# Kernel tuning notes

Measured on AMD Instinct MI355X. Metric: run time of the kernel, lower is better.

## Reference

```python
import jax, jax.numpy as jnp
import numpy as np

NUM_HEADS = 12
DIM = 1536
HEAD_DIM = DIM // NUM_HEADS
ROPE_BASE = 10000.0


def _alibi_slopes(n):
    import math
    def pow2_slopes(m):
        start = 2.0 ** (-(2.0 ** (-(math.log2(m) - 3))))
        return [start * (start ** i) for i in range(m)]
    if math.log2(n).is_integer():
        s = pow2_slopes(n)
    else:
        c = 2 ** math.floor(math.log2(n))
        s = pow2_slopes(c) + pow2_slopes(2 * c)[0::2][: n - c]
    return jnp.asarray(np.array(s, dtype=np.float32))


def _rope_tables(seq_len, head_dim, dtype):
    inv_freq = 1.0 / (ROPE_BASE ** (jnp.arange(0, head_dim, 2, dtype=jnp.float32) / head_dim))
    t = jnp.arange(seq_len, dtype=jnp.float32)
    freqs = jnp.outer(t, inv_freq)  # [S, head_dim/2]
    return jnp.cos(freqs).astype(dtype), jnp.sin(freqs).astype(dtype)


def _apply_rope(t, cos, sin):
    # t: [B,H,S,hd]; cos/sin: [S, hd/2] -> interleaved rotation
    te, to = t[..., 0::2], t[..., 1::2]
    rot = jnp.stack([te * cos - to * sin, te * sin + to * cos], axis=-1)
    return rot.reshape(t.shape)


def setup_inputs() -> dict:
    key = jax.random.key(0)
    ks = jax.random.split(key, 9)
    B, S, D = 2, 2048, DIM
    w_scale = 1.0 / np.sqrt(D)
    return {
        "x": jax.random.normal(ks[0], (B, S, D), dtype=jnp.float32),
        "Wq": jax.random.normal(ks[1], (D, D), dtype=jnp.float32) * w_scale,
        "bq": jnp.zeros((D,), dtype=jnp.float32),
        "Wk": jax.random.normal(ks[2], (D, D), dtype=jnp.float32) * w_scale,
        "bk": jnp.zeros((D,), dtype=jnp.float32),
        "Wv": jax.random.normal(ks[3], (D, D), dtype=jnp.float32) * w_scale,
        "bv": jnp.zeros((D,), dtype=jnp.float32),
        "Wo": jax.random.normal(ks[4], (D, D), dtype=jnp.float32) * w_scale,
        "bo": jnp.zeros((D,), dtype=jnp.float32),
    }


def reference(x, Wq, bq, Wk, bk, Wv, bv, Wo, bo):
    B, S, D = x.shape
    H, hd = NUM_HEADS, D // NUM_HEADS
    scale = hd ** -0.5

    def proj(W, b):
        # nn.Linear: x @ W.T + b ; reshape to [B,H,S,hd]
        y = jnp.einsum("bsd,ed->bse", x, W) + b
        return y.reshape(B, S, H, hd).transpose(0, 2, 1, 3)

    q, k, v = proj(Wq, bq), proj(Wk, bk), proj(Wv, bv)

    cos, sin = _rope_tables(S, hd, x.dtype)
    q = _apply_rope(q, cos, sin)
    k = _apply_rope(k, cos, sin)

    scores = jnp.einsum("bhqd,bhkd->bhqk", q, k) * scale
    slopes = _alibi_slopes(H)  # [H]
    # original bias: slopes * arange(seq_len) broadcast over key positions
    scores = scores + slopes[None, :, None, None] * jnp.arange(S, dtype=x.dtype)[None, None, None, :]

    attn = jax.nn.softmax(scores, axis=-1)  # dropout is identity at eval
    out = jnp.einsum("bhqk,bhkd->bhqd", attn, v)
    out = out.transpose(0, 2, 1, 3).reshape(B, S, D)
    return jnp.einsum("bsd,ed->bse", out, Wo) + bo
```

## Files before the change

### kernel.cpp

```cpp
#include <hip/hip_runtime.h>
#include <math.h>

#define S_LEN   2048
#define NHEADS  12
#define HD      128
#define DMODEL  1536
#define NBATCH  2

typedef __bf16 bf16x8 __attribute__((ext_vector_type(8)));
typedef float  f32x4  __attribute__((ext_vector_type(4)));
typedef unsigned short u16x8 __attribute__((ext_vector_type(8)));

__constant__ float c_slopes[NHEADS] = {
    0.5f, 0.25f, 0.125f, 0.0625f, 0.03125f, 0.015625f, 0.0078125f, 0.00390625f,
    0.70710678118654752f, 0.35355339059327379f,
    0.17677669529663689f, 0.08838834764831845f
};

__device__ __forceinline__ unsigned short f2bf(float x) {
    unsigned int u = __float_as_uint(x);
    u += 0x7FFFu + ((u >> 16) & 1u);
    return (unsigned short)(u >> 16);
}
__device__ __forceinline__ float bf2f(unsigned short h) {
    return __uint_as_float(((unsigned int)h) << 16);
}
__device__ __forceinline__ void splitf(float v, unsigned short &h, unsigned short &l) {
    h = f2bf(v);
    l = f2bf(v - bf2f(h));
}
__device__ __forceinline__ f32x4 mfma16(bf16x8 a, bf16x8 b, f32x4 c) {
    return __builtin_amdgcn_mfma_f32_16x16x32_bf16(a, b, c, 0, 0, 0);
}

__global__ void rope_table_kernel(float* __restrict__ cosT, float* __restrict__ sinT) {
    const int s = blockIdx.x;
    const int i = threadIdx.x;
    double inv = exp(-((double)i / 64.0) * 9.210340371976184);
    float argf = (float)s * (float)inv;
    double a = (double)argf;
    cosT[s * 64 + i] = (float)cos(a);
    sinT[s * 64 + i] = (float)sin(a);
}

__global__ __launch_bounds__(256)
void conv_hl_kernel(const float* __restrict__ src,
                    unsigned short* __restrict__ dh,
                    unsigned short* __restrict__ dl, int n8)
{
    int idx = blockIdx.x * 256 + threadIdx.x;
    if (idx >= n8) return;
    const float4* s = (const float4*)src + (size_t)idx * 2;
    float4 a = s[0], b = s[1];
    u16x8 hv, lv;
    unsigned short th, tl;
    splitf(a.x, th, tl); hv[0] = th; lv[0] = tl;
    splitf(a.y, th, tl); hv[1] = th; lv[1] = tl;
    splitf(a.z, th, tl); hv[2] = th; lv[2] = tl;
    splitf(a.w, th, tl); hv[3] = th; lv[3] = tl;
    splitf(b.x, th, tl); hv[4] = th; lv[4] = tl;
    splitf(b.y, th, tl); hv[5] = th; lv[5] = tl;
    splitf(b.z, th, tl); hv[6] = th; lv[6] = tl;
    splitf(b.w, th, tl); hv[7] = th; lv[7] = tl;
    *(u16x8*)(dh + (size_t)idx * 8) = hv;
    *(u16x8*)(dl + (size_t)idx * 8) = lv;
}

__global__ __launch_bounds__(256, 4)
void transpose_vt_kernel(const unsigned short* __restrict__ inH,
                         const unsigned short* __restrict__ inL,
                         unsigned short* __restrict__ outH,
                         unsigned short* __restrict__ outL)
{
    __shared__ unsigned short Th[64 * 65], Tl[64 * 65];
    const int tid = threadIdx.x;
    const int sx = blockIdx.x * 64, dx = blockIdx.y * 64;
    const int bh = blockIdx.z;
    const size_t ibase = (size_t)bh * S_LEN * HD;
    const size_t obase = (size_t)bh * HD * S_LEN;

#pragma unroll
    for (int t = 0; t < 2; t++) {
        int srow = (tid >> 3) + 32 * t;
        int c8 = tid & 7;
        u16x8 vh = *(const u16x8*)(inH + ibase + (size_t)(sx + srow) * HD + dx + c8 * 8);
        u16x8 vl = *(const u16x8*)(inL + ibase + (size_t)(sx + srow) * HD + dx + c8 * 8);
#pragma unroll
        for (int j = 0; j < 8; j++) {
            Th[(c8 * 8 + j) * 65 + srow] = vh[j];
            Tl[(c8 * 8 + j) * 65 + srow] = vl[j];
        }
    }
    __syncthreads();
#pragma unroll
    for (int t = 0; t < 2; t++) {
        int drow = (tid >> 3) + 32 * t;
        int c8 = tid & 7;
        u16x8 vh, vl;
#pragma unroll
        for (int j = 0; j < 8; j++) {
            vh[j] = Th[drow * 65 + c8 * 8 + j];
            vl[j] = Tl[drow * 65 + c8 * 8 + j];
        }
        *(u16x8*)(outH + obase + (size_t)(dx + drow) * S_LEN + sx + c8 * 8) = vh;
        *(u16x8*)(outL + obase + (size_t)(dx + drow) * S_LEN + sx + c8 * 8) = vl;
    }
}

#define BM 128
#define BN 128
#define BK 32
#define LDT 40

__global__ __launch_bounds__(256, 2)
void gemm_hl_kernel(const unsigned short* __restrict__ Agh, const unsigned short* __restrict__ Agl,
                    const unsigned short* __restrict__ Bgh, const unsigned short* __restrict__ Bgl,
                    int M, int N, int K,
                    float* __restrict__ outF, const float* __restrict__ bO,
                    unsigned short* __restrict__ Qh, unsigned short* __restrict__ Ql,
                    unsigned short* __restrict__ Kh, unsigned short* __restrict__ Kl,
                    unsigned short* __restrict__ Vh, unsigned short* __restrict__ Vl,
                    const float* __restrict__ bq, const float* __restrict__ bk,
                    const float* __restrict__ bv,
                    const float* __restrict__ cosT, const float* __restrict__ sinT,
                    int mode)
{
    __shared__ unsigned short Ah[BM * LDT], Al[BM * LDT];
    __shared__ unsigned short Bh[BN * LDT], Bl[BN * LDT];

    const int tid  = threadIdx.x;
    const int lane = tid & 63;
    const int wid  = tid >> 6;
    const int wm   = wid >> 1, wn = wid & 1;
    const int m0   = blockIdx.x * BM, n0 = blockIdx.y * BN;
    const int l15  = lane & 15, l4 = lane >> 4;
    const int kq   = l4 * 8;

    const int srow = tid >> 1, skc = (tid & 1) * 16;
    const size_t abase = (size_t)(m0 + srow) * K + skc;
    const size_t bbase = (size_t)(n0 + srow) * K + skc;

    f32x4 acc[4][4] = {};

    u16x8 pah0 = *(const u16x8*)(Agh + abase);
    u16x8 pah1 = *(const u16x8*)(Agh + abase + 8);
    u16x8 pal0 = *(const u16x8*)(Agl + abase);
    u16x8 pal1 = *(const u16x8*)(Agl + abase + 8);
    u16x8 pbh0 = *(const u16x8*)(Bgh + bbase);
    u16x8 pbh1 = *(const u16x8*)(Bgh + bbase + 8);
    u16x8 pbl0 = *(const u16x8*)(Bgl + bbase);
    u16x8 pbl1 = *(const u16x8*)(Bgl + bbase + 8);

    const int KT = K / BK;
    for (int kt = 0; kt < KT; ++kt) {
        __syncthreads();
        *(u16x8*)&Ah[srow * LDT + skc]     = pah0;
        *(u16x8*)&Ah[srow * LDT + skc + 8] = pah1;
        *(u16x8*)&Al[srow * LDT + skc]     = pal0;
        *(u16x8*)&Al[srow * LDT + skc + 8] = pal1;
        *(u16x8*)&Bh[srow * LDT + skc]     = pbh0;
        *(u16x8*)&Bh[srow * LDT + skc + 8] = pbh1;
        *(u16x8*)&Bl[srow * LDT + skc]     = pbl0;
        *(u16x8*)&Bl[srow * LDT + skc + 8] = pbl1;
        __syncthreads();

        if (kt + 1 < KT) {
            size_t ao = abase + (size_t)(kt + 1) * BK;
            size_t bo2 = bbase + (size_t)(kt + 1) * BK;
            pah0 = *(const u16x8*)(Agh + ao);
            pah1 = *(const u16x8*)(Agh + ao + 8);
            pal0 = *(const u16x8*)(Agl + ao);
            pal1 = *(const u16x8*)(Agl + ao + 8);
            pbh0 = *(const u16x8*)(Bgh + bo2);
            pbh1 = *(const u16x8*)(Bgh + bo2 + 8);
            pbl0 = *(const u16x8*)(Bgl + bo2);
            pbl1 = *(const u16x8*)(Bgl + bo2 + 8);
        }

        bf16x8 ah[4], al[4], bh[4], bl[4];
#pragma unroll
        for (int mi = 0; mi < 4; mi++) {
            int r = wm * 64 + mi * 16 + l15;
            ah[mi] = *(const bf16x8*)&Ah[r * LDT + kq];
            al[mi] = *(const bf16x8*)&Al[r * LDT + kq];
        }
#pragma unroll
        for (int ni = 0; ni < 4; ni++) {
            int r = wn * 64 + ni * 16 + l15;
            bh[ni] = *(const bf16x8*)&Bh[r * LDT + kq];
            bl[ni] = *(const bf16x8*)&Bl[r * LDT + kq];
        }
        __builtin_amdgcn_s_setprio(1);
#pragma unroll
        for (int mi = 0; mi < 4; mi++) {
#pragma unroll
            for (int ni = 0; ni < 4; ni++) {
                acc[mi][ni] = mfma16(ah[mi], bh[ni], acc[mi][ni]);
                acc[mi][ni] = mfma16(ah[mi], bl[ni], acc[mi][ni]);
                acc[mi][ni] = mfma16(al[mi], bh[ni], acc[mi][ni]);
            }
        }
        __builtin_amdgcn_s_setprio(0);
    }

#pragma unroll
    for (int ni = 0; ni < 4; ni++) {
        int col = n0 + wn * 64 + ni * 16 + l15;
        float bvv;
        unsigned short *dh = nullptr, *dl = nullptr;
        int colL = col, dorope = 0;
        if (mode == 0) {
            bvv = bO[col];
        } else {
            int which = col / 1536;
            colL = col - which * 1536;
            const float* bias = (which == 0) ? bq : (which == 1) ? bk : bv;
            dh = (which == 0) ? Qh : (which == 1) ? Kh : Vh;
            dl = (which == 0) ? Ql : (which == 1) ? Kl : Vl;
            dorope = (which < 2);
            bvv = bias[colL];
        }
        int hcol = colL >> 7;
        int d    = colL & (HD - 1);
#pragma unroll
        for (int mi = 0; mi < 4; mi++) {
#pragma unroll
            for (int r = 0; r < 4; r++) {
                int row = m0 + wm * 64 + mi * 16 + l4 * 4 + r;
                float v = acc[mi][ni][r] + bvv;
                if (mode == 0) {
                    outF[(size_t)row * N + col] = v;
                } else {
                    int bb = row >> 11;
                    int ss = row & (S_LEN - 1);
                    if (dorope) {
                        float p  = __shfl_xor(v, 1);
                        float cc = cosT[ss * 64 + (d >> 1)];
                        float sn = sinT[ss * 64 + (d >> 1)];
                        v = (d & 1) ? fmaf(p, sn, v * cc) : fmaf(-p, sn, v * cc);
                    }
                    unsigned short hh, ll;
                    splitf(v, hh, ll);
                    size_t o = ((size_t)(bb * NHEADS + hcol) * S_LEN + ss) * HD + d;
                    dh[o] = hh;
                    dl[o] = ll;
                }
            }
        }
    }
}

#define QB  64
#define KB  32
#define LKD 136
#define LVD 40
#define LPD 40

__global__ __launch_bounds__(256, 3)
void flash_kernel(const unsigned short* __restrict__ Qh, const unsigned short* __restrict__ Ql,
                  const unsigned short* __restrict__ Kh, const unsigned short* __restrict__ Kl,
                  const unsigned short* __restrict__ VTh, const unsigned short* __restrict__ VTl,
                  unsigned short* __restrict__ AOh, unsigned short* __restrict__ AOl)
{
    __shared__ unsigned short Ksh[KB * LKD], Ksl[KB * LKD];
    __shared__ unsigned short Vth[HD * LVD], Vtl[HD * LVD];
    __shared__ unsigned short Psh[4 * 16 * LPD], Psl[4 * 16 * LPD];

    const int tid  = threadIdx.x, lane = tid & 63, wid = tid >> 6;
    const int l15  = lane & 15, l4 = lane >> 4;
    const int kq   = l4 * 8;
    const int qt   = blockIdx.x, bh = blockIdx.y;
    const int b    = bh / NHEADS, h = bh % NHEADS;
    const float slope = c_slopes[h];
    const float scale = 0.088388347648318447f;

    const size_t base  = (size_t)bh * S_LEN * HD;
    const size_t vbase = (size_t)bh * HD * S_LEN;

    bf16x8 qfh[4], qfl[4];
    {
        const int qrow = qt * QB + wid * 16 + l15;
#pragma unroll
        for (int ks = 0; ks < 4; ks++) {
            size_t o = base + (size_t)qrow * HD + ks * 32 + kq;
            qfh[ks] = *(const bf16x8*)(Qh + o);
            qfl[ks] = *(const bf16x8*)(Ql + o);
        }
    }

    float m_r[4], l_r[4];
#pragma unroll
    for (int r = 0; r < 4; r++) { m_r[r] = -1e30f; l_r[r] = 0.0f; }
    f32x4 oacc[8] = {};

    unsigned short* Pmh = &Psh[wid * 16 * LPD];
    unsigned short* Pml = &Psl[wid * 16 * LPD];

    for (int it = 0; it < S_LEN / KB; ++it) {
        const int kt = (S_LEN / KB - 1) - it;
        __syncthreads();
#pragma unroll
        for (int i = 0; i < 2; i++) {
            int u = tid + 256 * i;
            int row = u >> 4, c8 = u & 15;
            size_t g = base + (size_t)(kt * KB + row) * HD + c8 * 8;
            *(u16x8*)&Ksh[row * LKD + c8 * 8] = *(const u16x8*)(Kh + g);
            *(u16x8*)&Ksl[row * LKD + c8 * 8] = *(const u16x8*)(Kl + g);
        }
#pragma unroll
        for (int i = 0; i < 2; i++) {
            int u = tid + 256 * i;
            int row = (u >> 2) & 127;
            int c = u & 3;
            size_t g = vbase + (size_t)row * S_LEN + kt * KB + c * 8;
            *(u16x8*)&Vth[row * LVD + c * 8] = *(const u16x8*)(VTh + g);
            *(u16x8*)&Vtl[row * LVD + c * 8] = *(const u16x8*)(VTl + g);
        }
        __syncthreads();

        f32x4 sc[2] = {};
        __builtin_amdgcn_s_setprio(1);
#pragma unroll
        for (int ks = 0; ks < 4; ks++) {
#pragma unroll
            for (int nf = 0; nf < 2; nf++) {
                int krow = nf * 16 + l15;
                bf16x8 kh = *(const bf16x8*)&Ksh[krow * LKD + ks * 32 + kq];
                bf16x8 kl = *(const bf16x8*)&Ksl[krow * LKD + ks * 32 + kq];
                sc[nf] = mfma16(qfh[ks], kh, sc[nf]);
                sc[nf] = mfma16(qfh[ks], kl, sc[nf]);
                sc[nf] = mfma16(qfl[ks], kh, sc[nf]);
            }
        }
        __builtin_amdgcn_s_setprio(0);

        float mnew[4];
        int grow = 0;
        const float bias0 = slope * (float)(kt * KB + l15);
        const float bias1 = slope * (float)(kt * KB + 16 + l15);
#pragma unroll
        for (int r = 0; r < 4; r++) {
            float s0 = fmaf(sc[0][r], scale, bias0);
            float s1 = fmaf(sc[1][r], scale, bias1);
            sc[0][r] = s0;
            sc[1][r] = s1;
            float mx = fmaxf(s0, s1);
            mx = fmaxf(mx, __shfl_xor(mx, 1));
            mx = fmaxf(mx, __shfl_xor(mx, 2));
            mx = fmaxf(mx, __shfl_xor(mx, 4));
            mx = fmaxf(mx, __shfl_xor(mx, 8));
            mnew[r] = fmaxf(m_r[r], mx);
            grow |= (mnew[r] > m_r[r]) ? 1 : 0;
        }
        if (__any(grow)) {
#pragma unroll
            for (int r = 0; r < 4; r++) {
                float corr = __expf(m_r[r] - mnew[r]);
                m_r[r] = mnew[r];
                l_r[r] *= corr;
#pragma unroll
                for (int nf = 0; nf < 8; nf++) oacc[nf][r] *= corr;
            }
        }
#pragma unroll
        for (int r = 0; r < 4; r++) {
            float p0 = __expf(sc[0][r] - m_r[r]);
            float p1 = __expf(sc[1][r] - m_r[r]);
            sc[0][r] = p0;
            sc[1][r] = p1;
            float rs = p0 + p1;
            rs += __shfl_xor(rs, 1);
            rs += __shfl_xor(rs, 2);
            rs += __shfl_xor(rs, 4);
            rs += __shfl_xor(rs, 8);
            l_r[r] += rs;
        }

#pragma unroll
        for (int nf = 0; nf < 2; nf++) {
#pragma unroll
            for (int r = 0; r < 4; r++) {
                unsigned short hh, ll;
                splitf(sc[nf][r], hh, ll);
                int row = l4 * 4 + r, col = nf * 16 + l15;
                Pmh[row * LPD + col] = hh;
                Pml[row * LPD + col] = ll;
            }
        }
        asm volatile("s_waitcnt lgkmcnt(0)" ::: "memory");
        __builtin_amdgcn_sched_barrier(0);

        bf16x8 ph = *(const bf16x8*)&Pmh[l15 * LPD + kq];
        bf16x8 pl = *(const bf16x8*)&Pml[l15 * LPD + kq];
        __builtin_amdgcn_s_setprio(1);
#pragma unroll
        for (int nf = 0; nf < 8; nf++) {
            int vrow = nf * 16 + l15;
            bf16x8 vh = *(const bf16x8*)&Vth[vrow * LVD + kq];
            bf16x8 vl = *(const bf16x8*)&Vtl[vrow * LVD + kq];
            oacc[nf] = mfma16(ph, vh, oacc[nf]);
            oacc[nf] = mfma16(ph, vl, oacc[nf]);
            oacc[nf] = mfma16(pl, vh, oacc[nf]);
        }
        __builtin_amdgcn_s_setprio(0);
    }

#pragma unroll
    for (int r = 0; r < 4; r++) {
        float inv = 1.0f / l_r[r];
        int srow = qt * QB + wid * 16 + l4 * 4 + r;
        size_t ob = ((size_t)b * S_LEN + srow) * DMODEL + h * HD;
#pragma unroll
        for (int nf = 0; nf < 8; nf++) {
            unsigned short hh, ll;
            splitf(oacc[nf][r] * inv, hh, ll);
            AOh[ob + nf * 16 + l15] = hh;
            AOl[ob + nf * 16 + l15] = ll;
        }
    }
}

extern "C" void kernel_launch(void* const* d_in, const int* in_sizes, int n_in,
                              void* d_out, int out_size, void* d_ws, size_t ws_size,
                              hipStream_t stream)
{
    const float* x  = (const float*)d_in[0];
    const float* Wq = (const float*)d_in[1];
    const float* bq = (const float*)d_in[2];
    const float* Wk = (const float*)d_in[3];
    const float* bk = (const float*)d_in[4];
    const float* Wv = (const float*)d_in[5];
    const float* bv = (const float*)d_in[6];
    const float* Wo = (const float*)d_in[7];
    const float* bo = (const float*)d_in[8];
    float* out = (float*)d_out;

    char* ws = (char*)d_ws;
    const size_t SZ = 12582912;

    float* cosT = (float*)ws;           ws += 524288;
    float* sinT = (float*)ws;           ws += 524288;
    unsigned short* Xh  = (unsigned short*)ws; ws += SZ;
    unsigned short* Xl  = (unsigned short*)ws; ws += SZ;
    unsigned short* Wch = (unsigned short*)ws; ws += 14155776;
    unsigned short* Wcl = (unsigned short*)ws; ws += 14155776;
    unsigned short* Qhp = (unsigned short*)ws; ws += SZ;
    unsigned short* Qlp = (unsigned short*)ws; ws += SZ;
    unsigned short* Khp = (unsigned short*)ws; ws += SZ;
    unsigned short* Klp = (unsigned short*)ws; ws += SZ;
    unsigned short* Vhp = (unsigned short*)ws; ws += SZ;
    unsigned short* Vlp = (unsigned short*)ws; ws += SZ;
    unsigned short* VTh = (unsigned short*)ws; ws += SZ;
    unsigned short* VTl = (unsigned short*)ws; ws += SZ;

    unsigned short* AOh = Xh;
    unsigned short* AOl = Xl;
    unsigned short* Woh = Wch;
    unsigned short* Wol = Wcl;

    const int M = NBATCH * S_LEN;
    const int NW = 1536 * 1536;

    rope_table_kernel<<<dim3(S_LEN), dim3(64), 0, stream>>>(cosT, sinT);

    conv_hl_kernel<<<dim3(M * DMODEL / 8 / 256), 256, 0, stream>>>(x, Xh, Xl, M * DMODEL / 8);
    conv_hl_kernel<<<dim3(NW / 8 / 256), 256, 0, stream>>>(Wq, Wch, Wcl, NW / 8);
    conv_hl_kernel<<<dim3(NW / 8 / 256), 256, 0, stream>>>(Wk, Wch + (size_t)NW, Wcl + (size_t)NW, NW / 8);
    conv_hl_kernel<<<dim3(NW / 8 / 256), 256, 0, stream>>>(Wv, Wch + (size_t)2 * NW, Wcl + (size_t)2 * NW, NW / 8);

    gemm_hl_kernel<<<dim3(M / BM, 4608 / BN), 256, 0, stream>>>(
        Xh, Xl, Wch, Wcl, M, 4608, DMODEL,
        nullptr, nullptr, Qhp, Qlp, Khp, Klp, Vhp, Vlp,
        bq, bk, bv, cosT, sinT, 1);

    transpose_vt_kernel<<<dim3(S_LEN / 64, HD / 64, NBATCH * NHEADS), 256, 0, stream>>>(
        Vhp, Vlp, VTh, VTl);

    conv_hl_kernel<<<dim3(NW / 8 / 256), 256, 0, stream>>>(Wo, Woh, Wol, NW / 8);

    flash_kernel<<<dim3(S_LEN / QB, NBATCH * NHEADS), 256, 0, stream>>>(
        Qhp, Qlp, Khp, Klp, VTh, VTl, AOh, AOl);

    gemm_hl_kernel<<<dim3(M / BM, DMODEL / BN), 256, 0, stream>>>(
        AOh, AOl, Woh, Wol, M, DMODEL, DMODEL,
        out, bo, nullptr, nullptr, nullptr, nullptr, nullptr, nullptr,
        nullptr, nullptr, nullptr, nullptr, nullptr, 0);
}
```

Before: 678.1 us.

## Load GEMM and attention tiles with direct global-to-LDS loads and XOR swizzle

Replaces the register-staged global loads plus LDS stores in the GEMM and attention kernels with global_load_lds 16-byte direct transfers. Unpadded tiles now use an XOR swizzle to avoid bank conflicts. The GEMM loses its register prefetch of the next tile, so load latency is no longer overlapped with compute, and its occupancy hint is raised from 2 to 3 blocks per CU. This cuts VGPR use and LDS write instructions, but loads now sit between barriers without prefetch.

```diff
diff --git a/kernel.cpp b/kernel.cpp
--- a/kernel.cpp
+++ b/kernel.cpp
@@ -31,6 +31,11 @@
 }
 __device__ __forceinline__ f32x4 mfma16(bf16x8 a, bf16x8 b, f32x4 c) {
     return __builtin_amdgcn_mfma_f32_16x16x32_bf16(a, b, c, 0, 0, 0);
+}
+__device__ __forceinline__ void gl_lds16(const void* g, void* l) {
+    __builtin_amdgcn_global_load_lds(
+        (const __attribute__((address_space(1))) unsigned int*)g,
+        (__attribute__((address_space(3))) unsigned int*)l, 16, 0, 0);
 }
 
 __global__ void rope_table_kernel(float* __restrict__ cosT, float* __restrict__ sinT) {
@@ -72,7 +77,7 @@
                          unsigned short* __restrict__ outH,
                          unsigned short* __restrict__ outL)
 {
-    __shared__ unsigned short Th[64 * 65], Tl[64 * 65];
+    __shared__ __align__(16) unsigned short Th[64 * 65], Tl[64 * 65];
     const int tid = threadIdx.x;
     const int sx = blockIdx.x * 64, dx = blockIdx.y * 64;
     const int bh = blockIdx.z;
@@ -110,9 +115,8 @@
 #define BM 128
 #define BN 128
 #define BK 32
-#define LDT 40
-
-__global__ __launch_bounds__(256, 2)
+
+__global__ __launch_bounds__(256, 3)
 void gemm_hl_kernel(const unsigned short* __restrict__ Agh, const unsigned short* __restrict__ Agl,
                     const unsigned short* __restrict__ Bgh, const unsigned short* __restrict__ Bgl,
                     int M, int N, int K,
@@ -125,70 +129,49 @@
                     const float* __restrict__ cosT, const float* __restrict__ sinT,
                     int mode)
 {
-    __shared__ unsigned short Ah[BM * LDT], Al[BM * LDT];
-    __shared__ unsigned short Bh[BN * LDT], Bl[BN * LDT];
+    __shared__ __align__(16) unsigned short Ah[BM * BK], Al[BM * BK];
+    __shared__ __align__(16) unsigned short Bh[BN * BK], Bl[BN * BK];
 
     const int tid  = threadIdx.x;
     const int lane = tid & 63;
-    const int wid  = tid >> 6;
-    const int wm   = wid >> 1, wn = wid & 1;
+    const int w    = tid >> 6;
+    const int wm   = w >> 1, wn = w & 1;
     const int m0   = blockIdx.x * BM, n0 = blockIdx.y * BN;
     const int l15  = lane & 15, l4 = lane >> 4;
-    const int kq   = l4 * 8;
-
-    const int srow = tid >> 1, skc = (tid & 1) * 16;
-    const size_t abase = (size_t)(m0 + srow) * K + skc;
-    const size_t bbase = (size_t)(n0 + srow) * K + skc;
+    const int swb  = ((l4 ^ ((l15 >> 1) & 3)) << 4);
 
     f32x4 acc[4][4] = {};
-
-    u16x8 pah0 = *(const u16x8*)(Agh + abase);
-    u16x8 pah1 = *(const u16x8*)(Agh + abase + 8);
-    u16x8 pal0 = *(const u16x8*)(Agl + abase);
-    u16x8 pal1 = *(const u16x8*)(Agl + abase + 8);
-    u16x8 pbh0 = *(const u16x8*)(Bgh + bbase);
-    u16x8 pbh1 = *(const u16x8*)(Bgh + bbase + 8);
-    u16x8 pbl0 = *(const u16x8*)(Bgl + bbase);
-    u16x8 pbl1 = *(const u16x8*)(Bgl + bbase + 8);
 
     const int KT = K / BK;
     for (int kt = 0; kt < KT; ++kt) {
         __syncthreads();
-        *(u16x8*)&Ah[srow * LDT + skc]     = pah0;
-        *(u16x8*)&Ah[srow * LDT + skc + 8] = pah1;
-        *(u16x8*)&Al[srow * LDT + skc]     = pal0;
-        *(u16x8*)&Al[srow * LDT + skc + 8] = pal1;
-        *(u16x8*)&Bh[srow * LDT + skc]     = pbh0;
-        *(u16x8*)&Bh[srow * LDT + skc + 8] = pbh1;
-        *(u16x8*)&Bl[srow * LDT + skc]     = pbl0;
-        *(u16x8*)&Bl[srow * LDT + skc + 8] = pbl1;
+#pragma unroll
+        for (int j = 0; j < 2; j++) {
+            int row  = w * 32 + j * 16 + (lane >> 2);
+            int slot = lane & 3;
+            int sw   = ((slot ^ ((row >> 1) & 3)) << 4);
+            size_t ao = ((size_t)(m0 + row) * K + (size_t)kt * BK) * 2 + sw;
+            size_t bo2 = ((size_t)(n0 + row) * K + (size_t)kt * BK) * 2 + sw;
+            int ldsb = w * 2048 + j * 1024;
+            gl_lds16((const char*)Agh + ao,  (char*)Ah + ldsb);
+            gl_lds16((const char*)Agl + ao,  (char*)Al + ldsb);
+            gl_lds16((const char*)Bgh + bo2, (char*)Bh + ldsb);
+            gl_lds16((const char*)Bgl + bo2, (char*)Bl + ldsb);
+        }
         __syncthreads();
-
-        if (kt + 1 < KT) {
-            size_t ao = abase + (size_t)(kt + 1) * BK;
-            size_t bo2 = bbase + (size_t)(kt + 1) * BK;
-            pah0 = *(const u16x8*)(Agh + ao);
-            pah1 = *(const u16x8*)(Agh + ao + 8);
-            pal0 = *(const u16x8*)(Agl + ao);
-            pal1 = *(const u16x8*)(Agl + ao + 8);
-            pbh0 = *(const u16x8*)(Bgh + bo2);
-            pbh1 = *(const u16x8*)(Bgh + bo2 + 8);
-            pbl0 = *(const u16x8*)(Bgl + bo2);
-            pbl1 = *(const u16x8*)(Bgl + bo2 + 8);
-        }
 
         bf16x8 ah[4], al[4], bh[4], bl[4];
 #pragma unroll
         for (int mi = 0; mi < 4; mi++) {
             int r = wm * 64 + mi * 16 + l15;
-            ah[mi] = *(const bf16x8*)&Ah[r * LDT + kq];
-            al[mi] = *(const bf16x8*)&Al[r * LDT + kq];
+            ah[mi] = *(const bf16x8*)((const char*)Ah + r * 64 + swb);
+            al[mi] = *(const bf16x8*)((const char*)Al + r * 64 + swb);
         }
 #pragma unroll
         for (int ni = 0; ni < 4; ni++) {
             int r = wn * 64 + ni * 16 + l15;
-            bh[ni] = *(const bf16x8*)&Bh[r * LDT + kq];
-            bl[ni] = *(const bf16x8*)&Bl[r * LDT + kq];
+            bh[ni] = *(const bf16x8*)((const char*)Bh + r * 64 + swb);
+            bl[ni] = *(const bf16x8*)((const char*)Bl + r * 64 + swb);
         }
         __builtin_amdgcn_s_setprio(1);
 #pragma unroll
@@ -252,8 +235,6 @@
 
 #define QB  64
 #define KB  32
-#define LKD 136
-#define LVD 40
 #define LPD 40
 
 __global__ __launch_bounds__(256, 3)
@@ -262,24 +243,26 @@
                   const unsigned short* __restrict__ VTh, const unsigned short* __restrict__ VTl,
                   unsigned short* __restrict__ AOh, unsigned short* __restrict__ AOl)
 {
-    __shared__ unsigned short Ksh[KB * LKD], Ksl[KB * LKD];
-    __shared__ unsigned short Vth[HD * LVD], Vtl[HD * LVD];
-    __shared__ unsigned short Psh[4 * 16 * LPD], Psl[4 * 16 * LPD];
-
-    const int tid  = threadIdx.x, lane = tid & 63, wid = tid >> 6;
+    __shared__ __align__(16) unsigned short Ksh[KB * HD], Ksl[KB * HD];
+    __shared__ __align__(16) unsigned short Vth[HD * KB], Vtl[HD * KB];
+    __shared__ __align__(16) unsigned short Psh[4 * 16 * LPD], Psl[4 * 16 * LPD];
+
+    const int tid  = threadIdx.x, lane = tid & 63, w = tid >> 6;
     const int l15  = lane & 15, l4 = lane >> 4;
     const int kq   = l4 * 8;
     const int qt   = blockIdx.x, bh = blockIdx.y;
     const int b    = bh / NHEADS, h = bh % NHEADS;
     const float slope = c_slopes[h];
     const float scale = 0.088388347648318447f;
+    const int swb  = ((l4 ^ ((l15 >> 1) & 3)) << 4);
+    const int swk  = ((l15 & 7) << 4);
 
     const size_t base  = (size_t)bh * S_LEN * HD;
     const size_t vbase = (size_t)bh * HD * S_LEN;
 
     bf16x8 qfh[4], qfl[4];
     {
-        const int qrow = qt * QB + wid * 16 + l15;
+        const int qrow = qt * QB + w * 16 + l15;
 #pragma unroll
         for (int ks = 0; ks < 4; ks++) {
             size_t o = base + (size_t)qrow * HD + ks * 32 + kq;
@@ -293,28 +276,30 @@
     for (int r = 0; r < 4; r++) { m_r[r] = -1e30f; l_r[r] = 0.0f; }
     f32x4 oacc[8] = {};
 
-    unsigned short* Pmh = &Psh[wid * 16 * LPD];
-    unsigned short* Pml = &Psl[wid * 16 * LPD];
+    unsigned short* Pmh = &Psh[w * 16 * LPD];
+    unsigned short* Pml = &Psl[w * 16 * LPD];
 
     for (int it = 0; it < S_LEN / KB; ++it) {
         const int kt = (S_LEN / KB - 1) - it;
         __syncthreads();
 #pragma unroll
-        for (int i = 0; i < 2; i++) {
-            int u = tid + 256 * i;
-            int row = u >> 4, c8 = u & 15;
-            size_t g = base + (size_t)(kt * KB + row) * HD + c8 * 8;
-            *(u16x8*)&Ksh[row * LKD + c8 * 8] = *(const u16x8*)(Kh + g);
-            *(u16x8*)&Ksl[row * LKD + c8 * 8] = *(const u16x8*)(Kl + g);
-        }
-#pragma unroll
-        for (int i = 0; i < 2; i++) {
-            int u = tid + 256 * i;
-            int row = (u >> 2) & 127;
-            int c = u & 3;
-            size_t g = vbase + (size_t)row * S_LEN + kt * KB + c * 8;
-            *(u16x8*)&Vth[row * LVD + c * 8] = *(const u16x8*)(VTh + g);
-            *(u16x8*)&Vtl[row * LVD + c * 8] = *(const u16x8*)(VTl + g);
+        for (int j = 0; j < 2; j++) {
+            {
+                int row  = w * 8 + j * 4 + (lane >> 4);
+                int innp = ((lane & 15) << 4) ^ ((row & 7) << 4);
+                size_t ko = (base + (size_t)(kt * KB + row) * HD) * 2 + innp;
+                int ldsb = w * 2048 + j * 1024;
+                gl_lds16((const char*)Kh + ko, (char*)Ksh + ldsb);
+                gl_lds16((const char*)Kl + ko, (char*)Ksl + ldsb);
+            }
+            {
+                int row = w * 32 + j * 16 + (lane >> 2);
+                int sw  = (((lane & 3) ^ ((row >> 1) & 3)) << 4);
+                size_t vo = (vbase + (size_t)row * S_LEN + (size_t)kt * KB) * 2 + sw;
+                int ldsb = w * 2048 + j * 1024;
+                gl_lds16((const char*)VTh + vo, (char*)Vth + ldsb);
+                gl_lds16((const char*)VTl + vo, (char*)Vtl + ldsb);
+            }
         }
         __syncthreads();
 
@@ -325,8 +310,9 @@
 #pragma unroll
             for (int nf = 0; nf < 2; nf++) {
                 int krow = nf * 16 + l15;
-                bf16x8 kh = *(const bf16x8*)&Ksh[krow * LKD + ks * 32 + kq];
-                bf16x8 kl = *(const bf16x8*)&Ksl[krow * LKD + ks * 32 + kq];
+                int kbyte = krow * 256 + ((ks * 64 + l4 * 16) ^ swk);
+                bf16x8 kh = *(const bf16x8*)((const char*)Ksh + kbyte);
+                bf16x8 kl = *(const bf16x8*)((const char*)Ksl + kbyte);
                 sc[nf] = mfma16(qfh[ks], kh, sc[nf]);
                 sc[nf] = mfma16(qfh[ks], kl, sc[nf]);
                 sc[nf] = mfma16(qfl[ks], kh, sc[nf]);
@@ -396,8 +382,8 @@
 #pragma unroll
         for (int nf = 0; nf < 8; nf++) {
             int vrow = nf * 16 + l15;
-            bf16x8 vh = *(const bf16x8*)&Vth[vrow * LVD + kq];
-            bf16x8 vl = *(const bf16x8*)&Vtl[vrow * LVD + kq];
+            bf16x8 vh = *(const bf16x8*)((const char*)Vth + vrow * 64 + swb);
+            bf16x8 vl = *(const bf16x8*)((const char*)Vtl + vrow * 64 + swb);
             oacc[nf] = mfma16(ph, vh, oacc[nf]);
             oacc[nf] = mfma16(ph, vl, oacc[nf]);
             oacc[nf] = mfma16(pl, vh, oacc[nf]);
@@ -408,7 +394,7 @@
 #pragma unroll
     for (int r = 0; r < 4; r++) {
         float inv = 1.0f / l_r[r];
-        int srow = qt * QB + wid * 16 + l4 * 4 + r;
+        int srow = qt * QB + w * 16 + l4 * 4 + r;
         size_t ob = ((size_t)b * S_LEN + srow) * DMODEL + h * HD;
 #pragma unroll
         for (int nf = 0; nf < 8; nf++) {
```

Measured after the change: 599.8 us. -11.5%, faster.
